# Kernel optimization log

Measured on AMD Instinct MI355X. Metric: run time of the kernel, lower is better.

The kernel has to match this reference:

```python
import jax, jax.numpy as jnp
import numpy as np

B, T, CI, AR, H, DO = 16, 1024, 512, 256, 1024, 80
LN_EPS = 1e-5


def _lstm_cell(x, h, c, Wih, Whh, bih, bhh):
    # torch.nn.LSTMCell math, gate order i, f, g, o
    gates = x @ Wih.T + bih + h @ Whh.T + bhh
    i, f, g, o = jnp.split(gates, 4, axis=-1)
    c2 = jax.nn.sigmoid(f) * c + jax.nn.sigmoid(i) * jnp.tanh(g)
    h2 = jax.nn.sigmoid(o) * jnp.tanh(c2)
    return h2, c2


def _layer_norm(x, g, b):
    mu = x.mean(-1, keepdims=True)
    var = x.var(-1, keepdims=True)
    return (x - mu) / jnp.sqrt(var + LN_EPS) * g + b


def setup_inputs() -> dict:
    key = jax.random.key(0)
    ks = jax.random.split(key, 32)
    s = 0.02
    d = {
        'cond': jax.random.normal(ks[0], (B, T, CI), jnp.float32),
        'targets': jax.random.normal(ks[1], (B, T, DO), jnp.float32),
        'target_mean': jax.random.normal(ks[2], (DO,), jnp.float32) * 0.1,
        'target_scale': 1.0 + 0.1 * jax.random.uniform(ks[3], (DO,), jnp.float32),
        # prenet: Linear(DO->AR)-ReLU, Linear(AR->AR)-ReLU (dropout rate 0)
        'Wpre1': jax.random.normal(ks[4], (AR, DO), jnp.float32) * s,
        'bpre1': jnp.zeros((AR,), jnp.float32),
        'Wpre2': jax.random.normal(ks[5], (AR, AR), jnp.float32) * s,
        'bpre2': jnp.zeros((AR,), jnp.float32),
        # layer 0: input CI+AR
        'Wih0': jax.random.normal(ks[6], (4 * H, CI + AR), jnp.float32) * s,
        'Whh0': jax.random.normal(ks[7], (4 * H, H), jnp.float32) * s,
        'bih0': jnp.zeros((4 * H,), jnp.float32),
        'bhh0': jnp.zeros((4 * H,), jnp.float32),
        'lng0': jnp.ones((H,), jnp.float32),
        'lnb0': jnp.zeros((H,), jnp.float32),
        'Wp0': jax.random.normal(ks[8], (H, H), jnp.float32) * s,
        'bp0': jnp.zeros((H,), jnp.float32),
        # layer 1: input H
        'Wih1': jax.random.normal(ks[9], (4 * H, H), jnp.float32) * s,
        'Whh1': jax.random.normal(ks[10], (4 * H, H), jnp.float32) * s,
        'bih1': jnp.zeros((4 * H,), jnp.float32),
        'bhh1': jnp.zeros((4 * H,), jnp.float32),
        'lng1': jnp.ones((H,), jnp.float32),
        'lnb1': jnp.zeros((H,), jnp.float32),
        'Wp1': jax.random.normal(ks[11], (H, H), jnp.float32) * s,
        'bp1': jnp.zeros((H,), jnp.float32),
        # output projection H -> DO
        'Wout': jax.random.normal(ks[12], (DO, H), jnp.float32) * s,
        'bout': jnp.zeros((DO,), jnp.float32),
    }
    return d


def reference(cond, targets, target_mean, target_scale,
              Wpre1, bpre1, Wpre2, bpre2,
              Wih0, Whh0, bih0, bhh0, lng0, lnb0, Wp0, bp0,
              Wih1, Whh1, bih1, bhh1, lng1, lnb1, Wp1, bp1,
              Wout, bout):
    Bb, Tt, _ = cond.shape
    # teacher forcing: prev_out at step t is normalized targets[t-1], zeros at t=0
    norm_t = (targets - target_mean) / target_scale           # (B,T,DO)
    prev = jnp.concatenate(
        [jnp.zeros((Bb, 1, norm_t.shape[-1]), norm_t.dtype), norm_t[:, :-1]], axis=1)
    # prenet (vectorized over all timesteps; dropout rate 0)
    hpre = jax.nn.relu(prev @ Wpre1.T + bpre1)
    ar = jax.nn.relu(hpre @ Wpre2.T + bpre2)                  # (B,T,AR)
    x_all = jnp.concatenate([cond, ar], axis=-1).transpose(1, 0, 2)  # (T,B,CI+AR)

    Hd = Whh0.shape[1]
    z0 = jnp.zeros((Bb, Hd), cond.dtype)
    init = (z0, z0, z0, z0)  # (z0, c0, z1, c1)

    def step(carry, x_t):
        za, ca, zb, cb = carry
        h0, ca = _lstm_cell(x_t, za, ca, Wih0, Whh0, bih0, bhh0)
        za = jnp.tanh(_layer_norm(h0, lng0, lnb0) @ Wp0.T + bp0)
        h1, cb = _lstm_cell(za, zb, cb, Wih1, Whh1, bih1, bhh1)
        zb = jnp.tanh(_layer_norm(h1, lng1, lnb1) @ Wp1.T + bp1)
        return (za, ca, zb, cb), zb

    _, zs = jax.lax.scan(step, init, x_all)                   # (T,B,H)
    predicted = (zs @ Wout.T + bout).transpose(1, 0, 2)       # (B,T,DO)
    return predicted
```

## Files before the change

### kernel.cpp

```cpp
#include <hip/hip_runtime.h>


typedef unsigned short u16;
typedef short bf16x8 __attribute__((ext_vector_type(8)));
typedef float f32x4 __attribute__((ext_vector_type(4)));
typedef int i32x4 __attribute__((ext_vector_type(4)));

#define MFMA16(a, b, c) __builtin_amdgcn_mfma_f32_16x16x32_bf16((a), (b), (c), 0, 0, 0)

__device__ __forceinline__ u16 f2bf(float x) {
  unsigned u = __float_as_uint(x);
  return (u16)((u + 0x7fffu + ((u >> 16) & 1u)) >> 16);
}
__device__ __forceinline__ float bf2f(u16 h) { return __uint_as_float(((unsigned)h) << 16); }
__device__ __forceinline__ float sigf(float x) { return 1.f / (1.f + __expf(-x)); }

__device__ __forceinline__ void gstore128(u16* p, i32x4 v) {
  asm volatile("global_store_dwordx4 %0, %1, off sc0 sc1" ::"v"((void*)p), "v"(v) : "memory");
}

__device__ __forceinline__ void load8s(bf16x8 d[8], const u16* p) {
#pragma unroll
  for (int c = 0; c < 8; c++) d[c] = *(const bf16x8*)(p + (c << 5));
}

__device__ __forceinline__ int ld8sum(const int* base) {
  int v0, v1, v2, v3, v4, v5, v6, v7;
  asm volatile(
      "global_load_dword %0, %8, off sc0 sc1\n\t"
      "global_load_dword %1, %8, off offset:128 sc0 sc1\n\t"
      "global_load_dword %2, %8, off offset:256 sc0 sc1\n\t"
      "global_load_dword %3, %8, off offset:384 sc0 sc1\n\t"
      "global_load_dword %4, %8, off offset:512 sc0 sc1\n\t"
      "global_load_dword %5, %8, off offset:640 sc0 sc1\n\t"
      "global_load_dword %6, %8, off offset:768 sc0 sc1\n\t"
      "global_load_dword %7, %8, off offset:896 sc0 sc1\n\t"
      "s_waitcnt vmcnt(0)"
      : "=&v"(v0), "=&v"(v1), "=&v"(v2), "=&v"(v3), "=&v"(v4), "=&v"(v5), "=&v"(v6), "=&v"(v7)
      : "v"((const void*)base)
      : "memory");
  return v0 + v1 + v2 + v3 + v4 + v5 + v6 + v7;
}

__device__ __forceinline__ void cbar(int* ctr, int e, int tid, int slot) {
  asm volatile("s_waitcnt vmcnt(0)" ::: "memory");
  __syncthreads();
  if (tid == 0) {
    atomicAdd(ctr + (slot << 5), 1);
    const int target = e << 7;
    for (;;) {
      if (ld8sum(ctr) >= target) break;
      __builtin_amdgcn_s_sleep(2);
    }
  }
  __syncthreads();
}

__device__ __forceinline__ void wait_c(const int* ctr, int target, int tid) {
  if (tid == 0) {
    for (;;) {
      if (ld8sum(ctr) >= target) break;
      __builtin_amdgcn_s_sleep(2);
    }
  }
  __syncthreads();
}

__global__ __launch_bounds__(256) void cvt(const float* __restrict__ s, u16* __restrict__ d, int n) {
  int i = (blockIdx.x * 256 + threadIdx.x) * 4;
  if (i < n) {
    float4 v = *(const float4*)(s + i);
    unsigned lo = (unsigned)f2bf(v.x) | ((unsigned)f2bf(v.y) << 16);
    unsigned hi = (unsigned)f2bf(v.z) | ((unsigned)f2bf(v.w) << 16);
    *(uint2*)(d + i) = make_uint2(lo, hi);
  }
}

__global__ __launch_bounds__(256) void cvt_wpre1(const float* __restrict__ s, u16* __restrict__ d) {
  int i = blockIdx.x * 256 + threadIdx.x;
  int r = i / 96, c = i - r * 96;
  d[i] = (c < 80) ? f2bf(s[r * 80 + c]) : (u16)0;
}

__global__ __launch_bounds__(256) void bsum(const float* __restrict__ a, const float* __restrict__ b,
                                            float* __restrict__ o) {
  int i = blockIdx.x * 256 + threadIdx.x;
  if (i < 4096) o[i] = a[i] + b[i];
}

__global__ __launch_bounds__(256) void pack_prev(const float* __restrict__ tg, const float* __restrict__ mean,
                                                 const float* __restrict__ scale, u16* __restrict__ prevp) {
  int i = blockIdx.x * 256 + threadIdx.x;
  int row = i / 96, c = i - row * 96;
  int t = row >> 4, b = row & 15;
  float v = 0.f;
  if (c < 80 && t > 0) v = (tg[((size_t)b * 1024 + (t - 1)) * 80 + c] - mean[c]) / scale[c];
  prevp[i] = f2bf(v);
}

__global__ __launch_bounds__(256) void pack_cond(const float* __restrict__ cond, u16* __restrict__ xall) {
  int i = (blockIdx.x * 256 + threadIdx.x) * 4;
  int row = i >> 9, c = i & 511;
  int t = row >> 4, b = row & 15;
  float4 v = *(const float4*)(cond + ((size_t)b * 1024 + t) * 512 + c);
  unsigned lo = (unsigned)f2bf(v.x) | ((unsigned)f2bf(v.y) << 16);
  unsigned hi = (unsigned)f2bf(v.z) | ((unsigned)f2bf(v.w) << 16);
  *(uint2*)(xall + (size_t)row * 768 + c) = make_uint2(lo, hi);
}

__global__ __launch_bounds__(256) void gemm_bt(const u16* __restrict__ A, int lda, const u16* __restrict__ B,
                                               int ldb, u16* __restrict__ C, int ldc,
                                               const float* __restrict__ bias, int K, int relu) {
  __shared__ u16 As[64 * 40];
  __shared__ u16 Bs[64 * 40];
  const int tid = threadIdx.x, lane = tid & 63, wv = tid >> 6;
  const int wr = wv >> 1, wc = wv & 1;
  const int m0 = blockIdx.x * 64, n0 = blockIdx.y * 64;
  const int lr = tid >> 2, lc = (tid & 3) * 8;
  f32x4 z = {0.f, 0.f, 0.f, 0.f};
  f32x4 acc[2][2] = {{z, z}, {z, z}};
  const u16* Ap = A + (size_t)(m0 + lr) * lda + lc;
  const u16* Bp = B + (size_t)(n0 + lr) * ldb + lc;
  for (int k0 = 0; k0 < K; k0 += 32) {
    int4 av = *(const int4*)(Ap + k0);
    int4 bv = *(const int4*)(Bp + k0);
    __syncthreads();
    *(int4*)(As + lr * 40 + lc) = av;
    *(int4*)(Bs + lr * 40 + lc) = bv;
    __syncthreads();
#pragma unroll
    for (int mi = 0; mi < 2; mi++) {
      bf16x8 af = *(const bf16x8*)(As + (wr * 32 + mi * 16 + (lane & 15)) * 40 + (lane >> 4) * 8);
#pragma unroll
      for (int ni = 0; ni < 2; ni++) {
        bf16x8 bf = *(const bf16x8*)(Bs + (wc * 32 + ni * 16 + (lane & 15)) * 40 + (lane >> 4) * 8);
        acc[mi][ni] = MFMA16(af, bf, acc[mi][ni]);
      }
    }
  }
#pragma unroll
  for (int mi = 0; mi < 2; mi++)
#pragma unroll
    for (int ni = 0; ni < 2; ni++) {
      int n = n0 + wc * 32 + ni * 16 + (lane & 15);
      float bs = bias ? bias[n] : 0.f;
#pragma unroll
      for (int r = 0; r < 4; r++) {
        int m = m0 + wr * 32 + mi * 16 + (lane >> 4) * 4 + r;
        float x = acc[mi][ni][r] + bs;
        if (relu) x = fmaxf(x, 0.f);
        C[(size_t)m * ldc + n] = f2bf(x);
      }
    }
}

__global__ __launch_bounds__(256) void out_proj(const u16* __restrict__ zs, const u16* __restrict__ Wb,
                                                const float* __restrict__ bout, float* __restrict__ out) {
  int wv = threadIdx.x >> 6, lane = threadIdx.x & 63;
  int tile = blockIdx.x * 4 + wv;
  int mt = tile / 5, nt = tile - mt * 5;
  int m0 = mt * 16, n0 = nt * 16;
  const u16* ap = zs + (size_t)(m0 + (lane & 15)) * 1024 + (lane >> 4) * 8;
  const u16* bp = Wb + (size_t)(n0 + (lane & 15)) * 1024 + (lane >> 4) * 8;
  f32x4 acc = {0.f, 0.f, 0.f, 0.f};
  for (int k = 0; k < 1024; k += 32) {
    bf16x8 a = *(const bf16x8*)(ap + k);
    bf16x8 b = *(const bf16x8*)(bp + k);
    acc = MFMA16(a, b, acc);
  }
  int n = n0 + (lane & 15);
  float bb = bout[n];
#pragma unroll
  for (int r = 0; r < 4; r++) {
    int m = m0 + (lane >> 4) * 4 + r;
    int t = m >> 4, b = m & 15;
    out[(size_t)b * 81920 + t * 80 + n] = acc[r] + bb;
  }
}

struct RecP {
  const u16 *g0, *whh0b, *wih1b, *whh1b, *wp0b, *wp1b;
  const float *b1s, *bp0, *bp1, *lng0, *lnb0, *lng1, *lnb1;
  u16 *zs, *za_all, *hall;
  int *ctr0, *ctr1;
};

#define SLICE 1032
#define OFF_PARTIAL 132096
#define OFF_GATES 140288
#define OFF_RED1 142336
#define OFF_RED2 143360
#define OFF_MUSIG 144384
#define OFF_C 144512
#define OFF_G0S 145024
#define OFF_HT 146048
#define SMEM_BYTES 146304

__global__ __launch_bounds__(256, 1) void recurrent(RecP p) {
  extern __shared__ char smem[];
  u16* wA = (u16*)smem;
  u16* wB = wA + 32 * SLICE;
  float* partial = (float*)(smem + OFF_PARTIAL);
  float* gates2 = (float*)(smem + OFF_GATES);
  float* red1 = (float*)(smem + OFF_RED1);
  float* red2 = (float*)(smem + OFF_RED2);
  float* musig = (float*)(smem + OFF_MUSIG);
  float* cs = (float*)(smem + OFF_C);
  u16* g0s = (u16*)(smem + OFF_G0S);
  u16* htile = (u16*)(smem + OFF_HT);

  const int w = blockIdx.x, tid = threadIdx.x;
  const int lane = tid & 63, wv = tid >> 6;
  const int bl = lane & 15, q = lane >> 4;
  const bool grp0 = (w < 128);
  const int wl = grp0 ? w : (w - 128);
  const int slot = wl & 7;
  int* ctr = grp0 ? p.ctr0 : p.ctr1;

  {
    int r = tid >> 3, kp = tid & 7;
    int gN = (r >> 3) * 1024 + (wl << 3) + (r & 7);
    const u16* srcA = grp0 ? p.whh0b : p.wih1b;
#pragma unroll
    for (int i = 0; i < 16; i++) {
      int k = kp * 128 + i * 8;
      *(int4*)(wA + r * SLICE + k) = *(const int4*)(srcA + (size_t)gN * 1024 + k);
    }
    if (!grp0) {
#pragma unroll
      for (int i = 0; i < 16; i++) {
        int k = kp * 128 + i * 8;
        *(int4*)(wB + r * SLICE + k) = *(const int4*)(p.whh1b + (size_t)gN * 1024 + k);
      }
    } else {
      int r2 = tid >> 4, kp2 = tid & 15;
      int4 z4 = make_int4(0, 0, 0, 0);
#pragma unroll
      for (int i = 0; i < 8; i++) {
        int k = kp2 * 64 + i * 8;
        int4 v = z4;
        if (r2 < 8) v = *(const int4*)(p.wp0b + (size_t)((wl << 3) + r2) * 1024 + k);
        *(int4*)(wB + r2 * SLICE + k) = v;
      }
    }
    if (tid < 128) cs[tid] = 0.f;
  }
  __syncthreads();

  const int nl0 = tid >> 4, be = tid & 15;
  const int gN0 = (nl0 >> 3) * 1024 + (wl << 3) + (nl0 & 7);
  const int gN1 = ((nl0 + 16) >> 3) * 1024 + (wl << 3) + ((nl0 + 16) & 7);
  const float bp0v = p.bp0[(wl << 3) + ((tid >> 4) & 7)];
  const float bp1v = p.bp1[(wl << 3) + ((tid >> 4) & 7)];
  const float b1a = p.b1s[gN0], b1b = p.b1s[gN1];
  const int g0i0 = (((nl0 >> 3) << 4) + be) * 8 + (nl0 & 7);
  const int g0i1 = ((((nl0 >> 3) + 2) << 4) + be) * 8 + (nl0 & 7);

  if (grp0) {
    i32x4 gcur = {0, 0, 0, 0}, gnext = {0, 0, 0, 0};
    if (tid < 64) {
      int g = tid >> 4, b = tid & 15;
      const u16* gp = p.g0 + (size_t)b * 4096 + g * 1024 + (wl << 3);
      asm volatile("global_load_dwordx4 %0, %1, off sc0 sc1\n\ts_waitcnt vmcnt(0)"
                   : "=&v"(gcur)
                   : "v"((const void*)gp)
                   : "memory");
    }

    for (int t = 0; t < 1024; ++t) {
      u16* hx0 = p.hall + (size_t)t * 65536;

      if (t > 0) {
        const u16* zap = p.za_all + (size_t)(t - 1) * 16384 + bl * 1024 + (wv << 8) + (q << 3);
        bf16x8 av[8];
        load8s(av, zap);
        f32x4 acc0 = {0.f, 0.f, 0.f, 0.f}, acc1 = acc0;
#pragma unroll
        for (int c = 0; c < 8; c++) {
          int k = (wv << 8) + (c << 5) + (q << 3);
          acc0 = MFMA16(av[c], *(const bf16x8*)(wA + bl * SLICE + k), acc0);
          acc1 = MFMA16(av[c], *(const bf16x8*)(wA + (16 + bl) * SLICE + k), acc1);
        }
        *(f32x4*)(partial + (wv << 9) + (bl << 4) + (q << 2)) = acc0;
        *(f32x4*)(partial + (wv << 9) + ((16 + bl) << 4) + (q << 2)) = acc1;
      }
      if (tid < 64) *(i32x4*)(g0s + (tid << 3)) = gcur;
      if (t < 1023 && tid < 64) {
        int g = tid >> 4, b = tid & 15;
        const u16* gp = p.g0 + (size_t)(((t + 1) << 4) | b) * 4096 + g * 1024 + (wl << 3);
        asm volatile("global_load_dwordx4 %0, %1, off sc0 sc1"
                     : "=&v"(gnext)
                     : "v"((const void*)gp)
                     : "memory");
      }
      __syncthreads();
      {
        float s0 = bf2f(g0s[g0i0]), s1 = bf2f(g0s[g0i1]);
        if (t > 0) {
          int e0 = tid, e1 = tid + 256;
          s0 += partial[e0] + partial[512 + e0] + partial[1024 + e0] + partial[1536 + e0];
          s1 += partial[e1] + partial[512 + e1] + partial[1024 + e1] + partial[1536 + e1];
        }
        gates2[tid] = s0;
        gates2[tid + 256] = s1;
      }
      __syncthreads();
      if (tid < 128) {
        int jj = tid >> 4, b = tid & 15;
        float xi = gates2[(jj)*16 + b];
        float xf = gates2[(8 + jj) * 16 + b];
        float xg = gates2[(16 + jj) * 16 + b];
        float xo = gates2[(24 + jj) * 16 + b];
        float c = cs[tid];
        float cn = sigf(xf) * c + sigf(xi) * tanhf(xg);
        cs[tid] = cn;
        htile[(b << 3) + jj] = f2bf(sigf(xo) * tanhf(cn));
      }
      __syncthreads();
      if (tid < 16) gstore128(hx0 + tid * 1024 + (wl << 3), *(const i32x4*)(htile + (tid << 3)));
      cbar(ctr, 2 * t + 1, tid, slot);

      {
        bf16x8 dv[8];
        load8s(dv, hx0 + bl * 1024 + (wv << 8) + (q << 3));
        float sm = 0.f, sq = 0.f;
#pragma unroll
        for (int i = 0; i < 8; i++)
#pragma unroll
          for (int j = 0; j < 8; j++) {
            float x = bf2f((u16)dv[i][j]);
            sm += x;
            sq += x * x;
          }
        red1[(bl << 4) + (wv << 2) + q] = sm;
        red2[(bl << 4) + (wv << 2) + q] = sq;
        __syncthreads();
        if (tid < 64) {
          int b2 = tid >> 2, g2 = tid & 3;
          float s = red1[b2 * 16 + g2 * 4] + red1[b2 * 16 + g2 * 4 + 1] + red1[b2 * 16 + g2 * 4 + 2] +
                    red1[b2 * 16 + g2 * 4 + 3];
          float qq = red2[b2 * 16 + g2 * 4] + red2[b2 * 16 + g2 * 4 + 1] + red2[b2 * 16 + g2 * 4 + 2] +
                     red2[b2 * 16 + g2 * 4 + 3];
          s += __shfl_xor(s, 1);
          s += __shfl_xor(s, 2);
          qq += __shfl_xor(qq, 1);
          qq += __shfl_xor(qq, 2);
          if (g2 == 0) {
            float mu = s * (1.f / 1024.f);
            float var = qq * (1.f / 1024.f) - mu * mu;
            musig[b2] = mu;
            musig[16 + b2] = rsqrtf(var + 1e-5f);
          }
        }
        __syncthreads();
        float mu = musig[bl], rs = musig[16 + bl];
        f32x4 acc = {0.f, 0.f, 0.f, 0.f};
#pragma unroll
        for (int c = 0; c < 8; c++) {
          int k = (wv << 8) + (c << 5) + (q << 3);
          float4 ga = *(const float4*)(p.lng0 + k);
          float4 gb = *(const float4*)(p.lng0 + k + 4);
          float4 ba = *(const float4*)(p.lnb0 + k);
          float4 bb = *(const float4*)(p.lnb0 + k + 4);
          bf16x8 a;
          a[0] = (short)f2bf((bf2f((u16)dv[c][0]) - mu) * rs * ga.x + ba.x);
          a[1] = (short)f2bf((bf2f((u16)dv[c][1]) - mu) * rs * ga.y + ba.y);
          a[2] = (short)f2bf((bf2f((u16)dv[c][2]) - mu) * rs * ga.z + ba.z);
          a[3] = (short)f2bf((bf2f((u16)dv[c][3]) - mu) * rs * ga.w + ba.w);
          a[4] = (short)f2bf((bf2f((u16)dv[c][4]) - mu) * rs * gb.x + bb.x);
          a[5] = (short)f2bf((bf2f((u16)dv[c][5]) - mu) * rs * gb.y + bb.y);
          a[6] = (short)f2bf((bf2f((u16)dv[c][6]) - mu) * rs * gb.z + bb.z);
          a[7] = (short)f2bf((bf2f((u16)dv[c][7]) - mu) * rs * gb.w + bb.w);
          acc = MFMA16(a, *(const bf16x8*)(wB + bl * SLICE + k), acc);
        }
        *(f32x4*)(partial + (wv << 8) + (bl << 4) + (q << 2)) = acc;
      }
      __syncthreads();
      if (tid < 128) {
        int nl = tid >> 4, b = tid & 15;
        float s = partial[nl * 16 + b] + partial[256 + nl * 16 + b] + partial[512 + nl * 16 + b] +
                  partial[768 + nl * 16 + b] + bp0v;
        htile[(b << 3) + nl] = f2bf(tanhf(s));
      }
      __syncthreads();
      if (tid < 16)
        gstore128(p.za_all + (size_t)t * 16384 + tid * 1024 + (wl << 3), *(const i32x4*)(htile + (tid << 3)));
      cbar(ctr, 2 * t + 2, tid, slot);
      gcur = gnext;
    }
  } else {
    for (int t = 0; t < 1024; ++t) {
      u16* hx = p.hall + (size_t)t * 65536;
      wait_c(p.ctr0, (2 * t + 2) << 7, tid);

      {
        const u16* zap = p.za_all + (size_t)t * 16384 + bl * 1024 + (wv << 8) + (q << 3);
        bf16x8 a1[8];
        load8s(a1, zap);
        f32x4 acc0 = {0.f, 0.f, 0.f, 0.f}, acc1 = acc0;
        if (t > 0) {
          const u16* zbp = p.hall + (size_t)(t - 1) * 65536 + 32768 + bl * 1024 + (wv << 8) + (q << 3);
          bf16x8 a2[8];
          load8s(a2, zbp);
#pragma unroll
          for (int c = 0; c < 8; c++) {
            int k = (wv << 8) + (c << 5) + (q << 3);
            acc0 = MFMA16(a1[c], *(const bf16x8*)(wA + bl * SLICE + k), acc0);
            acc1 = MFMA16(a1[c], *(const bf16x8*)(wA + (16 + bl) * SLICE + k), acc1);
            acc0 = MFMA16(a2[c], *(const bf16x8*)(wB + bl * SLICE + k), acc0);
            acc1 = MFMA16(a2[c], *(const bf16x8*)(wB + (16 + bl) * SLICE + k), acc1);
          }
        } else {
#pragma unroll
          for (int c = 0; c < 8; c++) {
            int k = (wv << 8) + (c << 5) + (q << 3);
            acc0 = MFMA16(a1[c], *(const bf16x8*)(wA + bl * SLICE + k), acc0);
            acc1 = MFMA16(a1[c], *(const bf16x8*)(wA + (16 + bl) * SLICE + k), acc1);
          }
        }
        *(f32x4*)(partial + (wv << 9) + (bl << 4) + (q << 2)) = acc0;
        *(f32x4*)(partial + (wv << 9) + ((16 + bl) << 4) + (q << 2)) = acc1;
      }
      __syncthreads();
      {
        int e0 = tid, e1 = tid + 256;
        float s0 = partial[e0] + partial[512 + e0] + partial[1024 + e0] + partial[1536 + e0] + b1a;
        float s1 = partial[e1] + partial[512 + e1] + partial[1024 + e1] + partial[1536 + e1] + b1b;
        gates2[e0] = s0;
        gates2[e1] = s1;
      }
      __syncthreads();
      if (tid < 128) {
        int jj = tid >> 4, b = tid & 15;
        float xi = gates2[(jj)*16 + b];
        float xf = gates2[(8 + jj) * 16 + b];
        float xg = gates2[(16 + jj) * 16 + b];
        float xo = gates2[(24 + jj) * 16 + b];
        float c = cs[tid];
        float cn = sigf(xf) * c + sigf(xi) * tanhf(xg);
        cs[tid] = cn;
        htile[(b << 3) + jj] = f2bf(sigf(xo) * tanhf(cn));
      }
      __syncthreads();
      if (tid < 16) gstore128(hx + 16384 + tid * 1024 + (wl << 3), *(const i32x4*)(htile + (tid << 3)));
      cbar(ctr, 2 * t + 1, tid, slot);

      {
        const u16* h1p = hx + 16384;
        bf16x8 dv[8];
        load8s(dv, h1p + bl * 1024 + (wv << 8) + (q << 3));
        float sm = 0.f, sq = 0.f;
#pragma unroll
        for (int i = 0; i < 8; i++)
#pragma unroll
          for (int j = 0; j < 8; j++) {
            float x = bf2f((u16)dv[i][j]);
            sm += x;
            sq += x * x;
          }
        red1[(bl << 4) + (wv << 2) + q] = sm;
        red2[(bl << 4) + (wv << 2) + q] = sq;
        __syncthreads();
        if (tid < 64) {
          int b2 = tid >> 2, g2 = tid & 3;
          float s = red1[b2 * 16 + g2 * 4] + red1[b2 * 16 + g2 * 4 + 1] + red1[b2 * 16 + g2 * 4 + 2] +
                    red1[b2 * 16 + g2 * 4 + 3];
          float qq = red2[b2 * 16 + g2 * 4] + red2[b2 * 16 + g2 * 4 + 1] + red2[b2 * 16 + g2 * 4 + 2] +
                     red2[b2 * 16 + g2 * 4 + 3];
          s += __shfl_xor(s, 1);
          s += __shfl_xor(s, 2);
          qq += __shfl_xor(qq, 1);
          qq += __shfl_xor(qq, 2);
          if (g2 == 0) {
            float mu = s * (1.f / 1024.f);
            float var = qq * (1.f / 1024.f) - mu * mu;
            musig[b2] = mu;
            musig[16 + b2] = rsqrtf(var + 1e-5f);
          }
        }
        __syncthreads();
        float mu = musig[bl], rs = musig[16 + bl];
        f32x4 acc = {0.f, 0.f, 0.f, 0.f};
        const u16* wpp = p.wp1b + (size_t)((wl << 3) + (bl & 7)) * 1024;
        bf16x8 z8 = {0, 0, 0, 0, 0, 0, 0, 0};
#pragma unroll
        for (int c = 0; c < 8; c++) {
          int k = (wv << 8) + (c << 5) + (q << 3);
          float4 ga = *(const float4*)(p.lng1 + k);
          float4 gb = *(const float4*)(p.lng1 + k + 4);
          float4 ba = *(const float4*)(p.lnb1 + k);
          float4 bb = *(const float4*)(p.lnb1 + k + 4);
          bf16x8 a;
          a[0] = (short)f2bf((bf2f((u16)dv[c][0]) - mu) * rs * ga.x + ba.x);
          a[1] = (short)f2bf((bf2f((u16)dv[c][1]) - mu) * rs * ga.y + ba.y);
          a[2] = (short)f2bf((bf2f((u16)dv[c][2]) - mu) * rs * ga.z + ba.z);
          a[3] = (short)f2bf((bf2f((u16)dv[c][3]) - mu) * rs * ga.w + ba.w);
          a[4] = (short)f2bf((bf2f((u16)dv[c][4]) - mu) * rs * gb.x + bb.x);
          a[5] = (short)f2bf((bf2f((u16)dv[c][5]) - mu) * rs * gb.y + bb.y);
          a[6] = (short)f2bf((bf2f((u16)dv[c][6]) - mu) * rs * gb.z + bb.z);
          a[7] = (short)f2bf((bf2f((u16)dv[c][7]) - mu) * rs * gb.w + bb.w);
          bf16x8 bw = *(const bf16x8*)(wpp + k);
          if (bl >= 8) bw = z8;
          acc = MFMA16(a, bw, acc);
        }
        *(f32x4*)(partial + (wv << 8) + (bl << 4) + (q << 2)) = acc;
      }
      __syncthreads();
      if (tid < 128) {
        int nl = tid >> 4, b = tid & 15;
        float s = partial[nl * 16 + b] + partial[256 + nl * 16 + b] + partial[512 + nl * 16 + b] +
                  partial[768 + nl * 16 + b] + bp1v;
        htile[(b << 3) + nl] = f2bf(tanhf(s));
      }
      __syncthreads();
      if (tid < 16) {
        i32x4 v = *(const i32x4*)(htile + (tid << 3));
        gstore128(hx + 32768 + tid * 1024 + (wl << 3), v);
        *(i32x4*)(p.zs + (size_t)((t << 4) | tid) * 1024 + (wl << 3)) = v;
      }
      cbar(ctr, 2 * t + 2, tid, slot);
    }
  }
}

extern "C" void kernel_launch(void* const* d_in, const int* in_sizes, int n_in, void* d_out, int out_size,
                              void* d_ws, size_t ws_size, hipStream_t stream) {
  const float* cond = (const float*)d_in[0];
  const float* targets = (const float*)d_in[1];
  const float* tmean = (const float*)d_in[2];
  const float* tscale = (const float*)d_in[3];
  const float* Wpre1 = (const float*)d_in[4];
  const float* bpre1 = (const float*)d_in[5];
  const float* Wpre2 = (const float*)d_in[6];
  const float* bpre2 = (const float*)d_in[7];
  const float* Wih0 = (const float*)d_in[8];
  const float* Whh0 = (const float*)d_in[9];
  const float* bih0 = (const float*)d_in[10];
  const float* bhh0 = (const float*)d_in[11];
  const float* lng0 = (const float*)d_in[12];
  const float* lnb0 = (const float*)d_in[13];
  const float* Wp0 = (const float*)d_in[14];
  const float* bp0 = (const float*)d_in[15];
  const float* Wih1 = (const float*)d_in[16];
  const float* Whh1 = (const float*)d_in[17];
  const float* bih1 = (const float*)d_in[18];
  const float* bhh1 = (const float*)d_in[19];
  const float* lng1 = (const float*)d_in[20];
  const float* lnb1 = (const float*)d_in[21];
  const float* Wp1 = (const float*)d_in[22];
  const float* bp1 = (const float*)d_in[23];
  const float* Wout = (const float*)d_in[24];
  const float* bout = (const float*)d_in[25];

  char* ws = (char*)d_ws;
  int* ctr0 = (int*)(ws + 0);
  int* ctr1 = (int*)(ws + 2048);
  float* b0s = (float*)(ws + 102400);
  float* b1s = (float*)(ws + 118784);
  u16* woutb = (u16*)(ws + 135168);
  u16* wpre1b = (u16*)(ws + 299008);
  u16* wpre2b = (u16*)(ws + 348160);
  u16* wih0b = (u16*)(ws + 479232);
  u16* whh0b = (u16*)(ws + 6770688);
  u16* wih1b = (u16*)(ws + 15159296);
  u16* whh1b = (u16*)(ws + 23547904);
  u16* wp0b = (u16*)(ws + 31936512);
  u16* wp1b = (u16*)(ws + 34033664);
  u16* prevp = (u16*)(ws + 36130816);
  u16* hpre = (u16*)(ws + 39276544);
  u16* xall = (u16*)(ws + 47665152);
  u16* g0 = (u16*)(ws + 72830976);
  u16* zs = (u16*)(ws + 207048704);
  u16* za_all = (u16*)(ws + 36130816);
  u16* hall = (u16*)(ws + 72699904);

  hipMemsetAsync(ws, 0, 4096, stream);

  cvt_wpre1<<<96, 256, 0, stream>>>(Wpre1, wpre1b);
  cvt<<<64, 256, 0, stream>>>(Wpre2, wpre2b, 65536);
  cvt<<<3072, 256, 0, stream>>>(Wih0, wih0b, 3145728);
  cvt<<<4096, 256, 0, stream>>>(Whh0, whh0b, 4194304);
  cvt<<<4096, 256, 0, stream>>>(Wih1, wih1b, 4194304);
  cvt<<<4096, 256, 0, stream>>>(Whh1, whh1b, 4194304);
  cvt<<<1024, 256, 0, stream>>>(Wp0, wp0b, 1048576);
  cvt<<<1024, 256, 0, stream>>>(Wp1, wp1b, 1048576);
  cvt<<<80, 256, 0, stream>>>(Wout, woutb, 81920);
  bsum<<<16, 256, 0, stream>>>(bih0, bhh0, b0s);
  bsum<<<16, 256, 0, stream>>>(bih1, bhh1, b1s);
  pack_prev<<<6144, 256, 0, stream>>>(targets, tmean, tscale, prevp);
  pack_cond<<<8192, 256, 0, stream>>>(cond, xall);

  gemm_bt<<<dim3(256, 4), 256, 0, stream>>>(prevp, 96, wpre1b, 96, hpre, 256, bpre1, 96, 1);
  gemm_bt<<<dim3(256, 4), 256, 0, stream>>>(hpre, 256, wpre2b, 256, xall + 512, 768, bpre2, 256, 1);
  gemm_bt<<<dim3(256, 64), 256, 0, stream>>>(xall, 768, wih0b, 768, g0, 4096, b0s, 768, 0);

  RecP rp;
  rp.g0 = g0;
  rp.whh0b = whh0b;
  rp.wih1b = wih1b;
  rp.whh1b = whh1b;
  rp.wp0b = wp0b;
  rp.wp1b = wp1b;
  rp.b1s = b1s;
  rp.bp0 = bp0;
  rp.bp1 = bp1;
  rp.lng0 = lng0;
  rp.lnb0 = lnb0;
  rp.lng1 = lng1;
  rp.lnb1 = lnb1;
  rp.zs = zs;
  rp.za_all = za_all;
  rp.hall = hall;
  rp.ctr0 = ctr0;
  rp.ctr1 = ctr1;

  hipFuncSetAttribute(reinterpret_cast<const void*>(recurrent), hipFuncAttributeMaxDynamicSharedMemorySize,
                      SMEM_BYTES);
  recurrent<<<dim3(256), dim3(256), SMEM_BYTES, stream>>>(rp);

  out_proj<<<1280, 256, 0, stream>>>(zs, woutb, bout, (float*)d_out);
}
```

Baseline: 10.80 ms.

## Replace atomic-counter grid barrier with per-block flag stores and wave-wide polling

The inter-block barrier changes from atomicAdd into 8 striped counters, polled by one thread, to one flag per block that is written with a plain store of the epoch. A full wavefront then polls all 128 flags in parallel and exits via __all. This removes atomic contention and the serialized 8-load sum from the per-step barrier, which runs twice per timestep over 1024 steps. The g0 prefetch also moves to wave 1 with an explicit vmcnt wait, and the counter region grows to 16KB per group with a larger memset.

```diff
diff --git a/kernel.cpp b/kernel.cpp
--- a/kernel.cpp
+++ b/kernel.cpp
@@ -24,45 +24,37 @@
   for (int c = 0; c < 8; c++) d[c] = *(const bf16x8*)(p + (c << 5));
 }
 
-__device__ __forceinline__ int ld8sum(const int* base) {
-  int v0, v1, v2, v3, v4, v5, v6, v7;
-  asm volatile(
-      "global_load_dword %0, %8, off sc0 sc1\n\t"
-      "global_load_dword %1, %8, off offset:128 sc0 sc1\n\t"
-      "global_load_dword %2, %8, off offset:256 sc0 sc1\n\t"
-      "global_load_dword %3, %8, off offset:384 sc0 sc1\n\t"
-      "global_load_dword %4, %8, off offset:512 sc0 sc1\n\t"
-      "global_load_dword %5, %8, off offset:640 sc0 sc1\n\t"
-      "global_load_dword %6, %8, off offset:768 sc0 sc1\n\t"
-      "global_load_dword %7, %8, off offset:896 sc0 sc1\n\t"
-      "s_waitcnt vmcnt(0)"
-      : "=&v"(v0), "=&v"(v1), "=&v"(v2), "=&v"(v3), "=&v"(v4), "=&v"(v5), "=&v"(v6), "=&v"(v7)
-      : "v"((const void*)base)
-      : "memory");
-  return v0 + v1 + v2 + v3 + v4 + v5 + v6 + v7;
-}
-
-__device__ __forceinline__ void cbar(int* ctr, int e, int tid, int slot) {
-  asm volatile("s_waitcnt vmcnt(0)" ::: "memory");
+__device__ __forceinline__ void poll128(const int* flags, int e, int tid) {
+  if (tid < 64) {
+    const int* q0 = flags + (tid << 5);
+    const int* q1 = flags + ((tid + 64) << 5);
+    for (;;) {
+      int a, b;
+      asm volatile(
+          "global_load_dword %0, %2, off sc0 sc1\n\t"
+          "global_load_dword %1, %3, off sc0 sc1\n\t"
+          "s_waitcnt vmcnt(0)"
+          : "=&v"(a), "=&v"(b)
+          : "v"((const void*)q0), "v"((const void*)q1)
+          : "memory");
+      if (__all((a >= e) & (b >= e))) break;
+      __builtin_amdgcn_s_sleep(1);
+    }
+  }
+}
+
+__device__ __forceinline__ void cbar(int* flags, int e, int tid, int wl) {
+  if (tid < 64) asm volatile("s_waitcnt vmcnt(0)" ::: "memory");
   __syncthreads();
-  if (tid == 0) {
-    atomicAdd(ctr + (slot << 5), 1);
-    const int target = e << 7;
-    for (;;) {
-      if (ld8sum(ctr) >= target) break;
-      __builtin_amdgcn_s_sleep(2);
-    }
-  }
+  if (tid == 0)
+    asm volatile("global_store_dword %0, %1, off sc0 sc1" ::"v"((void*)(flags + (wl << 5))), "v"(e)
+                 : "memory");
+  poll128(flags, e, tid);
   __syncthreads();
 }
 
-__device__ __forceinline__ void wait_c(const int* ctr, int target, int tid) {
-  if (tid == 0) {
-    for (;;) {
-      if (ld8sum(ctr) >= target) break;
-      __builtin_amdgcn_s_sleep(2);
-    }
-  }
+__device__ __forceinline__ void wait_c(const int* flags, int e, int tid) {
+  poll128(flags, e, tid);
   __syncthreads();
 }
 
@@ -214,7 +206,6 @@
   const int bl = lane & 15, q = lane >> 4;
   const bool grp0 = (w < 128);
   const int wl = grp0 ? w : (w - 128);
-  const int slot = wl & 7;
   int* ctr = grp0 ? p.ctr0 : p.ctr1;
 
   {
@@ -258,8 +249,8 @@
 
   if (grp0) {
     i32x4 gcur = {0, 0, 0, 0}, gnext = {0, 0, 0, 0};
-    if (tid < 64) {
-      int g = tid >> 4, b = tid & 15;
+    if (wv == 1) {
+      int g = (tid >> 4) & 3, b = tid & 15;
       const u16* gp = p.g0 + (size_t)b * 4096 + g * 1024 + (wl << 3);
       asm volatile("global_load_dwordx4 %0, %1, off sc0 sc1\n\ts_waitcnt vmcnt(0)"
                    : "=&v"(gcur)
@@ -284,9 +275,12 @@
         *(f32x4*)(partial + (wv << 9) + (bl << 4) + (q << 2)) = acc0;
         *(f32x4*)(partial + (wv << 9) + ((16 + bl) << 4) + (q << 2)) = acc1;
       }
-      if (tid < 64) *(i32x4*)(g0s + (tid << 3)) = gcur;
-      if (t < 1023 && tid < 64) {
-        int g = tid >> 4, b = tid & 15;
+      if (wv == 1) {
+        asm volatile("s_waitcnt vmcnt(0)" ::: "memory");
+        *(i32x4*)(g0s + ((tid & 63) << 3)) = gcur;
+      }
+      if (t < 1023 && wv == 1) {
+        int g = (tid >> 4) & 3, b = tid & 15;
         const u16* gp = p.g0 + (size_t)(((t + 1) << 4) | b) * 4096 + g * 1024 + (wl << 3);
         asm volatile("global_load_dwordx4 %0, %1, off sc0 sc1"
                      : "=&v"(gnext)
@@ -318,7 +312,7 @@
       }
       __syncthreads();
       if (tid < 16) gstore128(hx0 + tid * 1024 + (wl << 3), *(const i32x4*)(htile + (tid << 3)));
-      cbar(ctr, 2 * t + 1, tid, slot);
+      cbar(ctr, 2 * t + 1, tid, wl);
 
       {
         bf16x8 dv[8];
@@ -385,13 +379,13 @@
       __syncthreads();
       if (tid < 16)
         gstore128(p.za_all + (size_t)t * 16384 + tid * 1024 + (wl << 3), *(const i32x4*)(htile + (tid << 3)));
-      cbar(ctr, 2 * t + 2, tid, slot);
+      cbar(ctr, 2 * t + 2, tid, wl);
       gcur = gnext;
     }
   } else {
     for (int t = 0; t < 1024; ++t) {
       u16* hx = p.hall + (size_t)t * 65536;
-      wait_c(p.ctr0, (2 * t + 2) << 7, tid);
+      wait_c(p.ctr0, 2 * t + 2, tid);
 
       {
         const u16* zap = p.za_all + (size_t)t * 16384 + bl * 1024 + (wv << 8) + (q << 3);
@@ -443,7 +437,7 @@
       }
       __syncthreads();
       if (tid < 16) gstore128(hx + 16384 + tid * 1024 + (wl << 3), *(const i32x4*)(htile + (tid << 3)));
-      cbar(ctr, 2 * t + 1, tid, slot);
+      cbar(ctr, 2 * t + 1, tid, wl);
 
       {
         const u16* h1p = hx + 16384;
@@ -518,7 +512,7 @@
         gstore128(hx + 32768 + tid * 1024 + (wl << 3), v);
         *(i32x4*)(p.zs + (size_t)((t << 4) | tid) * 1024 + (wl << 3)) = v;
       }
-      cbar(ctr, 2 * t + 2, tid, slot);
+      cbar(ctr, 2 * t + 2, tid, wl);
     }
   }
 }
@@ -554,7 +548,7 @@
 
   char* ws = (char*)d_ws;
   int* ctr0 = (int*)(ws + 0);
-  int* ctr1 = (int*)(ws + 2048);
+  int* ctr1 = (int*)(ws + 16384);
   float* b0s = (float*)(ws + 102400);
   float* b1s = (float*)(ws + 118784);
   u16* woutb = (u16*)(ws + 135168);
@@ -574,7 +568,7 @@
   u16* za_all = (u16*)(ws + 36130816);
   u16* hall = (u16*)(ws + 72699904);
 
-  hipMemsetAsync(ws, 0, 4096, stream);
+  hipMemsetAsync(ws, 0, 32768, stream);
 
   cvt_wpre1<<<96, 256, 0, stream>>>(Wpre1, wpre1b);
   cvt<<<64, 256, 0, stream>>>(Wpre2, wpre2b, 65536);
```

After: 11.00 ms. No clear change (+1.8%).

## Replace all-poll grid barrier with leader-detect and broadcast flag release

Applied to the files above, without the earlier changes.

The cross-block barrier used to have every block atomically increment a striped counter and then poll all eight stripes until the total was reached. Now only block 0 of each group polls the counters. It then writes the epoch into 32 spread-out flag slots, and the other blocks spin on a single flag dword with a shorter sleep; group 1 waits on group 0's broadcast flags. The per-step g0 prefetch also moves from wave 0 to wave 1 with an explicit wait, to take it off the wave that runs the barrier. The goal is less polling traffic and lower barrier latency in the 1024-step recurrence, at the cost of an extra broadcast hop through one leader block.

```diff
diff --git a/kernel.cpp b/kernel.cpp
--- a/kernel.cpp
+++ b/kernel.cpp
@@ -42,26 +42,44 @@
   return v0 + v1 + v2 + v3 + v4 + v5 + v6 + v7;
 }
 
-__device__ __forceinline__ void cbar(int* ctr, int e, int tid, int slot) {
-  asm volatile("s_waitcnt vmcnt(0)" ::: "memory");
+__device__ __forceinline__ int ld1(const int* p) {
+  int v;
+  asm volatile("global_load_dword %0, %1, off sc0 sc1\n\ts_waitcnt vmcnt(0)"
+               : "=&v"(v)
+               : "v"((const void*)p)
+               : "memory");
+  return v;
+}
+
+__device__ __forceinline__ void bcast(int* da, int* db, int e) {
+#pragma unroll
+  for (int i = 0; i < 32; i++) {
+    asm volatile("global_store_dword %0, %1, off sc0 sc1" ::"v"((void*)(da + (i << 5))), "v"(e) : "memory");
+    asm volatile("global_store_dword %0, %1, off sc0 sc1" ::"v"((void*)(db + (i << 5))), "v"(e) : "memory");
+  }
+}
+
+__device__ __forceinline__ void cbar(int* ctr, int* da, int* db, int e, int tid, int wl) {
+  if (tid < 64) asm volatile("s_waitcnt vmcnt(0)" ::: "memory");
+  if (tid == 0) {
+    atomicAdd(ctr + ((wl & 7) << 5), 1);
+    if (wl == 0) {
+      const int target = e << 7;
+      while (ld8sum(ctr) < target) {
+      }
+      bcast(da, db, e);
+    } else {
+      const int* q = da + ((wl & 31) << 5);
+      while (ld1(q) < e) __builtin_amdgcn_s_sleep(1);
+    }
+  }
   __syncthreads();
+}
+
+__device__ __forceinline__ void wait_c(const int* dext, int e, int tid, int wl) {
   if (tid == 0) {
-    atomicAdd(ctr + (slot << 5), 1);
-    const int target = e << 7;
-    for (;;) {
-      if (ld8sum(ctr) >= target) break;
-      __builtin_amdgcn_s_sleep(2);
-    }
-  }
-  __syncthreads();
-}
-
-__device__ __forceinline__ void wait_c(const int* ctr, int target, int tid) {
-  if (tid == 0) {
-    for (;;) {
-      if (ld8sum(ctr) >= target) break;
-      __builtin_amdgcn_s_sleep(2);
-    }
+    const int* q = dext + ((wl & 31) << 5);
+    while (ld1(q) < e) __builtin_amdgcn_s_sleep(1);
   }
   __syncthreads();
 }
@@ -183,6 +201,7 @@
   const float *b1s, *bp0, *bp1, *lng0, *lnb0, *lng1, *lnb1;
   u16 *zs, *za_all, *hall;
   int *ctr0, *ctr1;
+  int *d0o, *d0e, *d1o;
 };
 
 #define SLICE 1032
@@ -214,8 +233,9 @@
   const int bl = lane & 15, q = lane >> 4;
   const bool grp0 = (w < 128);
   const int wl = grp0 ? w : (w - 128);
-  const int slot = wl & 7;
   int* ctr = grp0 ? p.ctr0 : p.ctr1;
+  int* dla = grp0 ? p.d0o : p.d1o;
+  int* dlb = grp0 ? p.d0e : p.d1o;
 
   {
     int r = tid >> 3, kp = tid & 7;
@@ -258,8 +278,8 @@
 
   if (grp0) {
     i32x4 gcur = {0, 0, 0, 0}, gnext = {0, 0, 0, 0};
-    if (tid < 64) {
-      int g = tid >> 4, b = tid & 15;
+    if (wv == 1) {
+      int g = (tid >> 4) & 3, b = tid & 15;
       const u16* gp = p.g0 + (size_t)b * 4096 + g * 1024 + (wl << 3);
       asm volatile("global_load_dwordx4 %0, %1, off sc0 sc1\n\ts_waitcnt vmcnt(0)"
                    : "=&v"(gcur)
@@ -284,9 +304,12 @@
         *(f32x4*)(partial + (wv << 9) + (bl << 4) + (q << 2)) = acc0;
         *(f32x4*)(partial + (wv << 9) + ((16 + bl) << 4) + (q << 2)) = acc1;
       }
-      if (tid < 64) *(i32x4*)(g0s + (tid << 3)) = gcur;
-      if (t < 1023 && tid < 64) {
-        int g = tid >> 4, b = tid & 15;
+      if (wv == 1) {
+        asm volatile("s_waitcnt vmcnt(0)" ::: "memory");
+        *(i32x4*)(g0s + ((tid & 63) << 3)) = gcur;
+      }
+      if (t < 1023 && wv == 1) {
+        int g = (tid >> 4) & 3, b = tid & 15;
         const u16* gp = p.g0 + (size_t)(((t + 1) << 4) | b) * 4096 + g * 1024 + (wl << 3);
         asm volatile("global_load_dwordx4 %0, %1, off sc0 sc1"
                      : "=&v"(gnext)
@@ -318,7 +341,7 @@
       }
       __syncthreads();
       if (tid < 16) gstore128(hx0 + tid * 1024 + (wl << 3), *(const i32x4*)(htile + (tid << 3)));
-      cbar(ctr, 2 * t + 1, tid, slot);
+      cbar(ctr, dla, dlb, 2 * t + 1, tid, wl);
 
       {
         bf16x8 dv[8];
@@ -385,13 +408,13 @@
       __syncthreads();
       if (tid < 16)
         gstore128(p.za_all + (size_t)t * 16384 + tid * 1024 + (wl << 3), *(const i32x4*)(htile + (tid << 3)));
-      cbar(ctr, 2 * t + 2, tid, slot);
+      cbar(ctr, dla, dlb, 2 * t + 2, tid, wl);
       gcur = gnext;
     }
   } else {
     for (int t = 0; t < 1024; ++t) {
       u16* hx = p.hall + (size_t)t * 65536;
-      wait_c(p.ctr0, (2 * t + 2) << 7, tid);
+      wait_c(p.d0e, 2 * t + 2, tid, wl);
 
       {
         const u16* zap = p.za_all + (size_t)t * 16384 + bl * 1024 + (wv << 8) + (q << 3);
@@ -443,7 +466,7 @@
       }
       __syncthreads();
       if (tid < 16) gstore128(hx + 16384 + tid * 1024 + (wl << 3), *(const i32x4*)(htile + (tid << 3)));
-      cbar(ctr, 2 * t + 1, tid, slot);
+      cbar(ctr, dla, dlb, 2 * t + 1, tid, wl);
 
       {
         const u16* h1p = hx + 16384;
@@ -518,7 +541,7 @@
         gstore128(hx + 32768 + tid * 1024 + (wl << 3), v);
         *(i32x4*)(p.zs + (size_t)((t << 4) | tid) * 1024 + (wl << 3)) = v;
       }
-      cbar(ctr, 2 * t + 2, tid, slot);
+      cbar(ctr, dla, dlb, 2 * t + 2, tid, wl);
     }
   }
 }
@@ -555,6 +578,9 @@
   char* ws = (char*)d_ws;
   int* ctr0 = (int*)(ws + 0);
   int* ctr1 = (int*)(ws + 2048);
+  int* d0o = (int*)(ws + 4096);
+  int* d0e = (int*)(ws + 8192);
+  int* d1o = (int*)(ws + 12288);
   float* b0s = (float*)(ws + 102400);
   float* b1s = (float*)(ws + 118784);
   u16* woutb = (u16*)(ws + 135168);
@@ -574,7 +600,7 @@
   u16* za_all = (u16*)(ws + 36130816);
   u16* hall = (u16*)(ws + 72699904);
 
-  hipMemsetAsync(ws, 0, 4096, stream);
+  hipMemsetAsync(ws, 0, 32768, stream);
 
   cvt_wpre1<<<96, 256, 0, stream>>>(Wpre1, wpre1b);
   cvt<<<64, 256, 0, stream>>>(Wpre2, wpre2b, 65536);
@@ -613,6 +639,9 @@
   rp.hall = hall;
   rp.ctr0 = ctr0;
   rp.ctr1 = ctr1;
+  rp.d0o = d0o;
+  rp.d0e = d0e;
+  rp.d1o = d1o;
 
   hipFuncSetAttribute(reinterpret_cast<const void*>(recurrent), hipFuncAttributeMaxDynamicSharedMemorySize,
                       SMEM_BYTES);
```

Result: slower. 11.41 ms (+5.6%).
